# Optimization experiments

Measured on AMD Instinct MI355X. Metric: run time of the kernel, lower is better.

## Reference

```python
import jax, jax.numpy as jnp
import numpy as np

N_NODES = 50000
N_EDGES = 800000
N_GRAPHS = 256
N_FEAT, N_HID, N_EMB = 128, 256, 256
BN_EPS = 1e-5
W_SCALE = 0.05  # keep activations well-scaled through 3 layers


def setup_inputs() -> dict:
    key = jax.random.key(0)
    ks = jax.random.split(key, 9)
    x = jax.random.normal(ks[0], (N_NODES, N_FEAT), jnp.float32)
    edge_index = jax.random.randint(ks[1], (2, N_EDGES), 0, N_NODES)
    batch = jnp.sort(jax.random.randint(ks[2], (N_NODES,), 0, N_GRAPHS))
    return {
        "x": x,
        "edge_index": edge_index,
        "batch": batch,
        "W1_0": jax.random.normal(ks[3], (N_FEAT, N_HID), jnp.float32) * W_SCALE,
        "W2_0": jax.random.normal(ks[4], (N_HID, N_HID), jnp.float32) * W_SCALE,
        "gamma0": jnp.ones((N_HID,), jnp.float32),
        "beta0": jnp.zeros((N_HID,), jnp.float32),
        "W1_1": jax.random.normal(ks[5], (N_HID, N_HID), jnp.float32) * W_SCALE,
        "W2_1": jax.random.normal(ks[6], (N_HID, N_HID), jnp.float32) * W_SCALE,
        "gamma1": jnp.ones((N_HID,), jnp.float32),
        "beta1": jnp.zeros((N_HID,), jnp.float32),
        "W1_2": jax.random.normal(ks[7], (N_HID, N_HID), jnp.float32) * W_SCALE,
        "W2_2": jax.random.normal(ks[8], (N_HID, N_EMB), jnp.float32) * W_SCALE,
    }


def _gin_conv(x, src, dst, W1, W2):
    # PyG GINConv, eps=0: nn((1+eps)*x_i + sum_{j in N(i)} x_j)
    agg = jax.ops.segment_sum(x[src], dst, num_segments=N_NODES)  # [N, d]
    h = x + agg
    return jax.nn.relu(h @ W1) @ W2  # Linear(bias=False) -> act -> Linear(bias=False)


def _batch_norm(h, gamma, beta):
    # BatchNorm1d in training mode: biased batch stats over nodes
    mean = jnp.mean(h, axis=0)
    var = jnp.var(h, axis=0)
    return (h - mean) * jax.lax.rsqrt(var + BN_EPS) * gamma + beta


def reference(x, edge_index, batch, W1_0, W2_0, gamma0, beta0,
              W1_1, W2_1, gamma1, beta1, W1_2, W2_2):
    src, dst = edge_index[0], edge_index[1]
    layers = [(W1_0, W2_0, gamma0, beta0), (W1_1, W2_1, gamma1, beta1)]
    xs = []
    h = x
    for W1, W2, g, b in layers:  # n_layers-1 conv+act+BN blocks
        h = jax.nn.relu(_gin_conv(h, src, dst, W1, W2))
        h = _batch_norm(h, g, b)
        xs.append(h)
    h = _gin_conv(h, src, dst, W1_2, W2_2)  # final conv: no act, no BN
    xs.append(h)
    xpool = jax.ops.segment_sum(h, batch, num_segments=N_GRAPHS)  # global_add_pool
    return xpool, jnp.concatenate(xs, axis=1)
```

## Files before the change

kernel.cpp:

```cpp
#include <hip/hip_runtime.h>
#include <stdint.h>

typedef unsigned int u32;
typedef unsigned short u16;

using s16x8 = __attribute__((ext_vector_type(8))) short;
using f32x4 = __attribute__((ext_vector_type(4))) float;

#define N_NODES_C 50000
#define N_EDGES_C 800000
#define N_GRAPHS_C 256
#define N_FEAT_C 128
#define N_HID_C 256

static __device__ __forceinline__ float bf2f(u16 u) {
  union { u32 u; float f; } c; c.u = ((u32)u) << 16; return c.f;
}
static __device__ __forceinline__ u16 f2bf(float f) {
  union { float f; u32 u; } c; c.f = f;
  u32 u = c.u;
  return (u16)((u + 0x7fffu + ((u >> 16) & 1u)) >> 16);
}

static __device__ __forceinline__ void gload_lds16(const u16* g, u16* l) {
  __builtin_amdgcn_global_load_lds(
      (const __attribute__((address_space(1))) unsigned int*)g,
      (__attribute__((address_space(3))) unsigned int*)l, 16, 0, 0);
}

__global__ void convt_all_kernel(const float* __restrict__ Wa, const float* __restrict__ Wb,
                                 const float* __restrict__ Wc, const float* __restrict__ Wd,
                                 const float* __restrict__ We, const float* __restrict__ Wf,
                                 u16* oa, u16* ob, u16* oc, u16* od, u16* oe, u16* of_) {
  int m = blockIdx.y;
  const float* W; u16* o; int K;
  switch (m) {
    case 0: W = Wa; o = oa; K = 128; break;
    case 1: W = Wb; o = ob; K = 256; break;
    case 2: W = Wc; o = oc; K = 256; break;
    case 3: W = Wd; o = od; K = 256; break;
    case 4: W = We; o = oe; K = 256; break;
    default: W = Wf; o = of_; K = 256; break;
  }
  int idx = blockIdx.x * 256 + threadIdx.x;
  if (idx >= K * 256) return;
  int n = idx / K, k = idx - n * K;
  o[idx] = f2bf(W[(size_t)k * 256 + n]);
}

__global__ void cvt4_kernel(const float* __restrict__ x, u16* __restrict__ xb, int n4) {
  int idx = blockIdx.x * 256 + threadIdx.x;
  if (idx >= n4) return;
  float4 v = reinterpret_cast<const float4*>(x)[idx];
  u32 lo = (u32)f2bf(v.x) | ((u32)f2bf(v.y) << 16);
  u32 hi = (u32)f2bf(v.z) | ((u32)f2bf(v.w) << 16);
  uint2 w; w.x = lo; w.y = hi;
  reinterpret_cast<uint2*>(xb)[idx] = w;
}

__global__ void count_kernel(const int* __restrict__ dst, int* __restrict__ cnt, int E) {
  int e = blockIdx.x * 256 + threadIdx.x;
  if (e < E) atomicAdd(&cnt[dst[e]], 1);
}

__global__ void scanA_kernel(const int* __restrict__ cnt, int* __restrict__ incl,
                             int* __restrict__ bsum, int n) {
  __shared__ int sd[1024];
  int i = blockIdx.x * 1024 + (int)threadIdx.x;
  int v = (i < n) ? cnt[i] : 0;
  sd[threadIdx.x] = v;
  __syncthreads();
  for (int off = 1; off < 1024; off <<= 1) {
    int t = ((int)threadIdx.x >= off) ? sd[threadIdx.x - off] : 0;
    __syncthreads();
    sd[threadIdx.x] += t;
    __syncthreads();
  }
  if (i < n) incl[i] = sd[threadIdx.x];
  if (threadIdx.x == 1023) bsum[blockIdx.x] = sd[1023];
}

__global__ void scanB_kernel(int* bsum, int nb, float* stats0, float* stats1) {
  int t = threadIdx.x;
  for (int i = t; i < 512; i += 64) { stats0[i] = 0.f; stats1[i] = 0.f; }
  if (t == 0) {
    int s = 0;
    for (int b = 0; b < nb; b++) { int v = bsum[b]; bsum[b] = s; s += v; }
  }
}

__global__ void scanC_kernel(const int* __restrict__ cnt, const int* __restrict__ incl,
                             const int* __restrict__ bsum, int* __restrict__ offs,
                             int* __restrict__ cursor, int n) {
  int i = blockIdx.x * 1024 + (int)threadIdx.x;
  if (i < n) {
    int e = incl[i] - cnt[i] + bsum[blockIdx.x];
    offs[i] = e;
    cursor[i] = e;
  }
  if (i == 0) offs[n] = N_EDGES_C;
}

__global__ void fill_kernel(const int* __restrict__ src, const int* __restrict__ dst,
                            int* __restrict__ cursor, int* __restrict__ csr, int E) {
  int e = blockIdx.x * 256 + threadIdx.x;
  if (e < E) {
    int p = atomicAdd(&cursor[dst[e]], 1);
    csr[p] = src[e];
  }
}

template <int D>
__global__ __launch_bounds__(256) void agg_kernel(const u16* __restrict__ xin,
                                                  const int* __restrict__ offs,
                                                  const int* __restrict__ csr,
                                                  u16* __restrict__ hout) {
  constexpr int LPE = D / 8;
  constexpr int EPW = 64 / LPE;
  int wid = threadIdx.x >> 6, lane = threadIdx.x & 63;
  int node = blockIdx.x * 4 + wid;
  if (node >= N_NODES_C) return;
  int sub = lane / LPE;
  int fl = lane % LPE;
  int f0 = fl * 8;
  float acc[8];
  if (sub == 0) {
    uint4 v = *reinterpret_cast<const uint4*>(xin + (size_t)node * D + f0);
    const u32* pv = reinterpret_cast<const u32*>(&v);
#pragma unroll
    for (int t = 0; t < 4; t++) {
      acc[2 * t] = bf2f((u16)pv[t]);
      acc[2 * t + 1] = bf2f((u16)(pv[t] >> 16));
    }
  } else {
#pragma unroll
    for (int t = 0; t < 8; t++) acc[t] = 0.f;
  }
  int e = offs[node] + sub;
  int e1 = offs[node + 1];
  if (EPW == 2) {
    for (; e + 3 * EPW < e1; e += 4 * EPW) {
      int s0 = csr[e], s1 = csr[e + EPW], s2 = csr[e + 2 * EPW], s3 = csr[e + 3 * EPW];
      uint4 v0 = *reinterpret_cast<const uint4*>(xin + (size_t)s0 * D + f0);
      uint4 v1 = *reinterpret_cast<const uint4*>(xin + (size_t)s1 * D + f0);
      uint4 v2 = *reinterpret_cast<const uint4*>(xin + (size_t)s2 * D + f0);
      uint4 v3 = *reinterpret_cast<const uint4*>(xin + (size_t)s3 * D + f0);
      const u32* p0 = reinterpret_cast<const u32*>(&v0);
      const u32* p1 = reinterpret_cast<const u32*>(&v1);
      const u32* p2 = reinterpret_cast<const u32*>(&v2);
      const u32* p3 = reinterpret_cast<const u32*>(&v3);
#pragma unroll
      for (int t = 0; t < 4; t++) {
        acc[2 * t] += (bf2f((u16)p0[t]) + bf2f((u16)p1[t])) +
                      (bf2f((u16)p2[t]) + bf2f((u16)p3[t]));
        acc[2 * t + 1] += (bf2f((u16)(p0[t] >> 16)) + bf2f((u16)(p1[t] >> 16))) +
                          (bf2f((u16)(p2[t] >> 16)) + bf2f((u16)(p3[t] >> 16)));
      }
    }
  } else {
    for (; e + EPW < e1; e += 2 * EPW) {
      int s0 = csr[e], s1 = csr[e + EPW];
      uint4 v0 = *reinterpret_cast<const uint4*>(xin + (size_t)s0 * D + f0);
      uint4 v1 = *reinterpret_cast<const uint4*>(xin + (size_t)s1 * D + f0);
      const u32* p0 = reinterpret_cast<const u32*>(&v0);
      const u32* p1 = reinterpret_cast<const u32*>(&v1);
#pragma unroll
      for (int t = 0; t < 4; t++) {
        acc[2 * t] += bf2f((u16)p0[t]) + bf2f((u16)p1[t]);
        acc[2 * t + 1] += bf2f((u16)(p0[t] >> 16)) + bf2f((u16)(p1[t] >> 16));
      }
    }
  }
  for (; e < e1; e += EPW) {
    int s = csr[e];
    uint4 v = *reinterpret_cast<const uint4*>(xin + (size_t)s * D + f0);
    const u32* pv = reinterpret_cast<const u32*>(&v);
#pragma unroll
    for (int t = 0; t < 4; t++) {
      acc[2 * t] += bf2f((u16)pv[t]);
      acc[2 * t + 1] += bf2f((u16)(pv[t] >> 16));
    }
  }
#pragma unroll
  for (int j = 0; j < 8; j++) {
    if (EPW == 4) acc[j] += __shfl_xor(acc[j], 16, 64);
    acc[j] += __shfl_xor(acc[j], 32, 64);
  }
  if (sub == 0) {
    u32 w[4];
#pragma unroll
    for (int t = 0; t < 4; t++)
      w[t] = (u32)f2bf(acc[2 * t]) | ((u32)f2bf(acc[2 * t + 1]) << 16);
    *reinterpret_cast<uint4*>(hout + (size_t)node * D + f0) =
        *reinterpret_cast<const uint4*>(w);
  }
}

template <int K, bool RELU, bool OUTF32, bool STATS>
__global__ __launch_bounds__(256, 4) void gemm_kernel(const u16* __restrict__ A,
                                                      const u16* __restrict__ Bt,
                                                      u16* __restrict__ outB,
                                                      float* __restrict__ outF, int ldc,
                                                      float* __restrict__ statsp) {
  constexpr int BM = 64, BK = 64;
  __shared__ u16 Al[BM * BK];
  __shared__ u16 Bl[256 * BK];
  const int tid = threadIdx.x;
  const int wid = tid >> 6, lane = tid & 63;
  const int brow = blockIdx.x * BM;
  const int wc = wid * 64;
  f32x4 acc[4][4] = {};

  const int lrow = lane >> 3;
  const int lw = lane & 7;
  const int colA = (lw ^ lrow) * 8;
  const int sw = (lane & 7) << 3;

  for (int k0 = 0; k0 < K; k0 += BK) {
#pragma unroll
    for (int i = 0; i < 10; i++) {
      int c = wid * 10 + i;
      if (c < 8) {
        int r = c * 8 + lrow;
        int gr = brow + r;
        gr = gr < N_NODES_C ? gr : N_NODES_C - 1;
        gload_lds16(A + (size_t)gr * K + k0 + colA, &Al[c * 512]);
      } else {
        int cc = c - 8;
        int r = cc * 8 + lrow;
        gload_lds16(Bt + (size_t)r * K + k0 + colA, &Bl[cc * 512]);
      }
    }
    __syncthreads();
#pragma unroll
    for (int ks = 0; ks < BK; ks += 32) {
      const int kk = ks + (lane >> 4) * 8;
      const int ki = kk ^ sw;
      s16x8 a[4], b[4];
#pragma unroll
      for (int m = 0; m < 4; m++)
        a[m] = *reinterpret_cast<const s16x8*>(&Al[(m * 16 + (lane & 15)) * 64 + ki]);
#pragma unroll
      for (int n = 0; n < 4; n++)
        b[n] = *reinterpret_cast<const s16x8*>(&Bl[(wc + n * 16 + (lane & 15)) * 64 + ki]);
#pragma unroll
      for (int m = 0; m < 4; m++)
#pragma unroll
        for (int n = 0; n < 4; n++)
          acc[m][n] = __builtin_amdgcn_mfma_f32_16x16x32_bf16(a[m], b[n], acc[m][n], 0, 0, 0);
    }
    __syncthreads();
  }

  const int cb = wc + (lane & 15);
  const int rsub = (lane >> 4) * 4;
  float s1[4] = {0.f, 0.f, 0.f, 0.f}, s2[4] = {0.f, 0.f, 0.f, 0.f};
#pragma unroll
  for (int m = 0; m < 4; m++) {
#pragma unroll
    for (int r = 0; r < 4; r++) {
      int row = brow + m * 16 + rsub + r;
      if (row >= N_NODES_C) continue;
#pragma unroll
      for (int n = 0; n < 4; n++) {
        float v = acc[m][n][r];
        if (RELU) v = v > 0.f ? v : 0.f;
        int col = cb + n * 16;
        if (OUTF32)
          outF[(size_t)row * ldc + col] = v;
        else
          outB[(size_t)row * ldc + col] = f2bf(v);
        if (STATS) { s1[n] += v; s2[n] += v * v; }
      }
    }
  }
  if (STATS) {
#pragma unroll
    for (int n = 0; n < 4; n++) {
      float a0 = s1[n], b0 = s2[n];
      a0 += __shfl_xor(a0, 16, 64);
      b0 += __shfl_xor(b0, 16, 64);
      a0 += __shfl_xor(a0, 32, 64);
      b0 += __shfl_xor(b0, 32, 64);
      if (lane < 16) {
        atomicAdd(&statsp[cb + n * 16], a0);
        atomicAdd(&statsp[256 + cb + n * 16], b0);
      }
    }
  }
}

__global__ __launch_bounds__(256) void norm_kernel(const u16* __restrict__ xp,
                                                   const float* __restrict__ stats,
                                                   const float* __restrict__ gamma,
                                                   const float* __restrict__ beta,
                                                   float* __restrict__ cout,
                                                   u16* __restrict__ xn) {
  const float invM = 1.0f / (float)N_NODES_C;
  int f0 = (threadIdx.x & 127) * 2;
  int half = threadIdx.x >> 7;
  float m0 = stats[f0] * invM, m1 = stats[f0 + 1] * invM;
  float v0 = stats[256 + f0] * invM - m0 * m0;
  float v1 = stats[256 + f0 + 1] * invM - m1 * m1;
  float sc0 = gamma[f0] * rsqrtf(v0 + 1e-5f);
  float sc1 = gamma[f0 + 1] * rsqrtf(v1 + 1e-5f);
  float bi0 = beta[f0] - m0 * sc0;
  float bi1 = beta[f0 + 1] - m1 * sc1;
  for (int r = blockIdx.x * 2 + half; r < N_NODES_C; r += 2 * gridDim.x) {
    u32 w = *reinterpret_cast<const u32*>(xp + (size_t)r * 256 + f0);
    float y0 = fmaf(bf2f((u16)w), sc0, bi0);
    float y1 = fmaf(bf2f((u16)(w >> 16)), sc1, bi1);
    float2 y; y.x = y0; y.y = y1;
    *reinterpret_cast<float2*>(cout + (size_t)r * 768 + f0) = y;
    *reinterpret_cast<u32*>(xn + (size_t)r * 256 + f0) =
        (u32)f2bf(y0) | ((u32)f2bf(y1) << 16);
  }
}

__global__ __launch_bounds__(256) void pool_kernel(const float* __restrict__ c, int ldc,
                                                   const int* __restrict__ batch,
                                                   float* __restrict__ outp) {
  __shared__ float red[1024];
  int g = blockIdx.x;
  int wid = threadIdx.x >> 6, lane = threadIdx.x & 63;
  int lo = 0, hi = N_NODES_C;
  while (lo < hi) { int mid = (lo + hi) >> 1; if (batch[mid] < g) lo = mid + 1; else hi = mid; }
  int start = lo;
  hi = N_NODES_C;
  while (lo < hi) { int mid = (lo + hi) >> 1; if (batch[mid] <= g) lo = mid + 1; else hi = mid; }
  int end = lo;
  float acc[4] = {0.f, 0.f, 0.f, 0.f};
  for (int r = start + wid; r < end; r += 4) {
    float4 v = *reinterpret_cast<const float4*>(c + (size_t)r * ldc + lane * 4);
    acc[0] += v.x; acc[1] += v.y; acc[2] += v.z; acc[3] += v.w;
  }
#pragma unroll
  for (int j = 0; j < 4; j++) red[wid * 256 + lane * 4 + j] = acc[j];
  __syncthreads();
  int f = threadIdx.x;
  float s = red[f] + red[256 + f] + red[512 + f] + red[768 + f];
  outp[(size_t)g * 256 + f] = s;
}

extern "C" void kernel_launch(void* const* d_in, const int* in_sizes, int n_in,
                              void* d_out, int out_size, void* d_ws, size_t ws_size,
                              hipStream_t stream) {
  (void)in_sizes; (void)n_in; (void)out_size; (void)ws_size;
  const float* x = (const float*)d_in[0];
  const int* ei = (const int*)d_in[1];
  const int* batch = (const int*)d_in[2];
  const float* W1_0 = (const float*)d_in[3];
  const float* W2_0 = (const float*)d_in[4];
  const float* gamma0 = (const float*)d_in[5];
  const float* beta0 = (const float*)d_in[6];
  const float* W1_1 = (const float*)d_in[7];
  const float* W2_1 = (const float*)d_in[8];
  const float* gamma1 = (const float*)d_in[9];
  const float* beta1 = (const float*)d_in[10];
  const float* W1_2 = (const float*)d_in[11];
  const float* W2_2 = (const float*)d_in[12];

  float* out = (float*)d_out;
  float* xpool = out;
  float* concat = out + (size_t)N_GRAPHS_C * N_HID_C;

  char* ws = (char*)d_ws;
  size_t off = 0;
  auto alloc = [&](size_t bytes) -> char* {
    char* p = ws + off;
    off = (off + bytes + 255) & ~(size_t)255;
    return p;
  };
  int* cnt = (int*)alloc((N_NODES_C + 1) * 4);
  int* offs = (int*)alloc((N_NODES_C + 1) * 4);
  int* cursor = (int*)alloc(N_NODES_C * 4);
  int* incl = (int*)alloc(N_NODES_C * 4);
  int* bsum = (int*)alloc(64 * 4);
  int* csr = (int*)alloc((size_t)N_EDGES_C * 4);
  u16* xb = (u16*)alloc((size_t)N_NODES_C * N_FEAT_C * 2);
  u16* hin = (u16*)alloc((size_t)N_NODES_C * N_HID_C * 2);
  u16* tbuf = (u16*)alloc((size_t)N_NODES_C * N_HID_C * 2);
  u16* xn = (u16*)alloc((size_t)N_NODES_C * N_HID_C * 2);
  u16* w10t = (u16*)alloc((size_t)N_FEAT_C * N_HID_C * 2);
  u16* w20t = (u16*)alloc((size_t)N_HID_C * N_HID_C * 2);
  u16* w11t = (u16*)alloc((size_t)N_HID_C * N_HID_C * 2);
  u16* w21t = (u16*)alloc((size_t)N_HID_C * N_HID_C * 2);
  u16* w12t = (u16*)alloc((size_t)N_HID_C * N_HID_C * 2);
  u16* w22t = (u16*)alloc((size_t)N_HID_C * N_HID_C * 2);
  float* stats0 = (float*)alloc(512 * 4);
  float* stats1 = (float*)alloc(512 * 4);

  const int* srcv = ei;
  const int* dstv = ei + N_EDGES_C;
  const int nb = (N_NODES_C + 1023) / 1024;
  const int ggrid = (N_NODES_C + 63) / 64;

  hipMemsetAsync(cnt, 0, (N_NODES_C + 1) * 4, stream);

  convt_all_kernel<<<dim3(256, 6), 256, 0, stream>>>(W1_0, W2_0, W1_1, W2_1, W1_2, W2_2,
                                                     w10t, w20t, w11t, w21t, w12t, w22t);
  cvt4_kernel<<<(N_NODES_C * N_FEAT_C / 4 + 255) / 256, 256, 0, stream>>>(
      x, xb, N_NODES_C * N_FEAT_C / 4);

  count_kernel<<<(N_EDGES_C + 255) / 256, 256, 0, stream>>>(dstv, cnt, N_EDGES_C);
  scanA_kernel<<<nb, 1024, 0, stream>>>(cnt, incl, bsum, N_NODES_C);
  scanB_kernel<<<1, 64, 0, stream>>>(bsum, nb, stats0, stats1);
  scanC_kernel<<<nb, 1024, 0, stream>>>(cnt, incl, bsum, offs, cursor, N_NODES_C);
  fill_kernel<<<(N_EDGES_C + 255) / 256, 256, 0, stream>>>(srcv, dstv, cursor, csr, N_EDGES_C);

  agg_kernel<128><<<(N_NODES_C + 3) / 4, 256, 0, stream>>>(xb, offs, csr, hin);
  gemm_kernel<128, true, false, false><<<ggrid, 256, 0, stream>>>(hin, w10t, tbuf, nullptr, N_HID_C, nullptr);
  gemm_kernel<256, true, false, true><<<ggrid, 256, 0, stream>>>(tbuf, w20t, hin, nullptr, N_HID_C, stats0);
  norm_kernel<<<2048, 256, 0, stream>>>(hin, stats0, gamma0, beta0, concat + 0, xn);

  agg_kernel<256><<<(N_NODES_C + 3) / 4, 256, 0, stream>>>(xn, offs, csr, hin);
  gemm_kernel<256, true, false, false><<<ggrid, 256, 0, stream>>>(hin, w11t, tbuf, nullptr, N_HID_C, nullptr);
  gemm_kernel<256, true, false, true><<<ggrid, 256, 0, stream>>>(tbuf, w21t, hin, nullptr, N_HID_C, stats1);
  norm_kernel<<<2048, 256, 0, stream>>>(hin, stats1, gamma1, beta1, concat + 256, xn);

  agg_kernel<256><<<(N_NODES_C + 3) / 4, 256, 0, stream>>>(xn, offs, csr, hin);
  gemm_kernel<256, true, false, false><<<ggrid, 256, 0, stream>>>(hin, w12t, tbuf, nullptr, N_HID_C, nullptr);
  gemm_kernel<256, false, true, false><<<ggrid, 256, 0, stream>>>(tbuf, w22t, nullptr, concat + 512, 768, nullptr);

  pool_kernel<<<N_GRAPHS_C, 256, 0, stream>>>(concat + 512, 768, batch, xpool);
}
```

Measured before the change: 483.6 us.

## Fold BatchNorm affine into aggregation and enlarge GEMM tile to 128 rows

After: 455.2 us. 5.9% less time.

```diff
diff --git a/kernel.cpp b/kernel.cpp
--- a/kernel.cpp
+++ b/kernel.cpp
@@ -110,10 +110,11 @@
   }
 }
 
-template <int D>
+template <int D, bool AFFINE>
 __global__ __launch_bounds__(256) void agg_kernel(const u16* __restrict__ xin,
                                                   const int* __restrict__ offs,
                                                   const int* __restrict__ csr,
+                                                  const float* __restrict__ sb,
                                                   u16* __restrict__ hout) {
   constexpr int LPE = D / 8;
   constexpr int EPW = 64 / LPE;
@@ -136,8 +137,9 @@
 #pragma unroll
     for (int t = 0; t < 8; t++) acc[t] = 0.f;
   }
-  int e = offs[node] + sub;
+  int e0 = offs[node];
   int e1 = offs[node + 1];
+  int e = e0 + sub;
   if (EPW == 2) {
     for (; e + 3 * EPW < e1; e += 4 * EPW) {
       int s0 = csr[e], s1 = csr[e + EPW], s2 = csr[e + 2 * EPW], s3 = csr[e + 3 * EPW];
@@ -187,6 +189,17 @@
     acc[j] += __shfl_xor(acc[j], 32, 64);
   }
   if (sub == 0) {
+    if (AFFINE) {
+      float dp1 = (float)(e1 - e0 + 1);
+      float4 sca = *reinterpret_cast<const float4*>(sb + f0);
+      float4 scb = *reinterpret_cast<const float4*>(sb + f0 + 4);
+      float4 bia = *reinterpret_cast<const float4*>(sb + 256 + f0);
+      float4 bib = *reinterpret_cast<const float4*>(sb + 256 + f0 + 4);
+      float sc[8] = {sca.x, sca.y, sca.z, sca.w, scb.x, scb.y, scb.z, scb.w};
+      float bi[8] = {bia.x, bia.y, bia.z, bia.w, bib.x, bib.y, bib.z, bib.w};
+#pragma unroll
+      for (int j = 0; j < 8; j++) acc[j] = fmaf(acc[j], sc[j], bi[j] * dp1);
+    }
     u32 w[4];
 #pragma unroll
     for (int t = 0; t < 4; t++)
@@ -197,18 +210,19 @@
 }
 
 template <int K, bool RELU, bool OUTF32, bool STATS>
-__global__ __launch_bounds__(256, 4) void gemm_kernel(const u16* __restrict__ A,
+__global__ __launch_bounds__(512, 2) void gemm_kernel(const u16* __restrict__ A,
                                                       const u16* __restrict__ Bt,
                                                       u16* __restrict__ outB,
                                                       float* __restrict__ outF, int ldc,
                                                       float* __restrict__ statsp) {
-  constexpr int BM = 64, BK = 64;
+  constexpr int BM = 128, BK = 64;
   __shared__ u16 Al[BM * BK];
   __shared__ u16 Bl[256 * BK];
   const int tid = threadIdx.x;
   const int wid = tid >> 6, lane = tid & 63;
   const int brow = blockIdx.x * BM;
-  const int wc = wid * 64;
+  const int wr = (wid >> 2) * 64;
+  const int wc = (wid & 3) * 64;
   f32x4 acc[4][4] = {};
 
   const int lrow = lane >> 3;
@@ -218,15 +232,15 @@
 
   for (int k0 = 0; k0 < K; k0 += BK) {
 #pragma unroll
-    for (int i = 0; i < 10; i++) {
-      int c = wid * 10 + i;
-      if (c < 8) {
+    for (int i = 0; i < 6; i++) {
+      int c = wid * 6 + i;
+      if (c < 16) {
         int r = c * 8 + lrow;
         int gr = brow + r;
         gr = gr < N_NODES_C ? gr : N_NODES_C - 1;
         gload_lds16(A + (size_t)gr * K + k0 + colA, &Al[c * 512]);
       } else {
-        int cc = c - 8;
+        int cc = c - 16;
         int r = cc * 8 + lrow;
         gload_lds16(Bt + (size_t)r * K + k0 + colA, &Bl[cc * 512]);
       }
@@ -239,7 +253,7 @@
       s16x8 a[4], b[4];
 #pragma unroll
       for (int m = 0; m < 4; m++)
-        a[m] = *reinterpret_cast<const s16x8*>(&Al[(m * 16 + (lane & 15)) * 64 + ki]);
+        a[m] = *reinterpret_cast<const s16x8*>(&Al[(wr + m * 16 + (lane & 15)) * 64 + ki]);
 #pragma unroll
       for (int n = 0; n < 4; n++)
         b[n] = *reinterpret_cast<const s16x8*>(&Bl[(wc + n * 16 + (lane & 15)) * 64 + ki]);
@@ -259,7 +273,7 @@
   for (int m = 0; m < 4; m++) {
 #pragma unroll
     for (int r = 0; r < 4; r++) {
-      int row = brow + m * 16 + rsub + r;
+      int row = brow + wr + m * 16 + rsub + r;
       if (row >= N_NODES_C) continue;
 #pragma unroll
       for (int n = 0; n < 4; n++) {
@@ -295,7 +309,7 @@
                                                    const float* __restrict__ gamma,
                                                    const float* __restrict__ beta,
                                                    float* __restrict__ cout,
-                                                   u16* __restrict__ xn) {
+                                                   float* __restrict__ sb) {
   const float invM = 1.0f / (float)N_NODES_C;
   int f0 = (threadIdx.x & 127) * 2;
   int half = threadIdx.x >> 7;
@@ -306,14 +320,16 @@
   float sc1 = gamma[f0 + 1] * rsqrtf(v1 + 1e-5f);
   float bi0 = beta[f0] - m0 * sc0;
   float bi1 = beta[f0 + 1] - m1 * sc1;
+  if (blockIdx.x == 0 && half == 0) {
+    sb[f0] = sc0; sb[f0 + 1] = sc1;
+    sb[256 + f0] = bi0; sb[256 + f0 + 1] = bi1;
+  }
   for (int r = blockIdx.x * 2 + half; r < N_NODES_C; r += 2 * gridDim.x) {
     u32 w = *reinterpret_cast<const u32*>(xp + (size_t)r * 256 + f0);
     float y0 = fmaf(bf2f((u16)w), sc0, bi0);
     float y1 = fmaf(bf2f((u16)(w >> 16)), sc1, bi1);
     float2 y; y.x = y0; y.y = y1;
     *reinterpret_cast<float2*>(cout + (size_t)r * 768 + f0) = y;
-    *reinterpret_cast<u32*>(xn + (size_t)r * 256 + f0) =
-        (u32)f2bf(y0) | ((u32)f2bf(y1) << 16);
   }
 }
 
@@ -380,7 +396,7 @@
   u16* xb = (u16*)alloc((size_t)N_NODES_C * N_FEAT_C * 2);
   u16* hin = (u16*)alloc((size_t)N_NODES_C * N_HID_C * 2);
   u16* tbuf = (u16*)alloc((size_t)N_NODES_C * N_HID_C * 2);
-  u16* xn = (u16*)alloc((size_t)N_NODES_C * N_HID_C * 2);
+  u16* hpre = (u16*)alloc((size_t)N_NODES_C * N_HID_C * 2);
   u16* w10t = (u16*)alloc((size_t)N_FEAT_C * N_HID_C * 2);
   u16* w20t = (u16*)alloc((size_t)N_HID_C * N_HID_C * 2);
   u16* w11t = (u16*)alloc((size_t)N_HID_C * N_HID_C * 2);
@@ -389,11 +405,13 @@
   u16* w22t = (u16*)alloc((size_t)N_HID_C * N_HID_C * 2);
   float* stats0 = (float*)alloc(512 * 4);
   float* stats1 = (float*)alloc(512 * 4);
+  float* sb0 = (float*)alloc(512 * 4);
+  float* sb1 = (float*)alloc(512 * 4);
 
   const int* srcv = ei;
   const int* dstv = ei + N_EDGES_C;
   const int nb = (N_NODES_C + 1023) / 1024;
-  const int ggrid = (N_NODES_C + 63) / 64;
+  const int ggrid = (N_NODES_C + 127) / 128;
 
   hipMemsetAsync(cnt, 0, (N_NODES_C + 1) * 4, stream);
 
@@ -408,19 +426,19 @@
   scanC_kernel<<<nb, 1024, 0, stream>>>(cnt, incl, bsum, offs, cursor, N_NODES_C);
   fill_kernel<<<(N_EDGES_C + 255) / 256, 256, 0, stream>>>(srcv, dstv, cursor, csr, N_EDGES_C);
 
-  agg_kernel<128><<<(N_NODES_C + 3) / 4, 256, 0, stream>>>(xb, offs, csr, hin);
-  gemm_kernel<128, true, false, false><<<ggrid, 256, 0, stream>>>(hin, w10t, tbuf, nullptr, N_HID_C, nullptr);
-  gemm_kernel<256, true, false, true><<<ggrid, 256, 0, stream>>>(tbuf, w20t, hin, nullptr, N_HID_C, stats0);
-  norm_kernel<<<2048, 256, 0, stream>>>(hin, stats0, gamma0, beta0, concat + 0, xn);
-
-  agg_kernel<256><<<(N_NODES_C + 3) / 4, 256, 0, stream>>>(xn, offs, csr, hin);
-  gemm_kernel<256, true, false, false><<<ggrid, 256, 0, stream>>>(hin, w11t, tbuf, nullptr, N_HID_C, nullptr);
-  gemm_kernel<256, true, false, true><<<ggrid, 256, 0, stream>>>(tbuf, w21t, hin, nullptr, N_HID_C, stats1);
-  norm_kernel<<<2048, 256, 0, stream>>>(hin, stats1, gamma1, beta1, concat + 256, xn);
-
-  agg_kernel<256><<<(N_NODES_C + 3) / 4, 256, 0, stream>>>(xn, offs, csr, hin);
-  gemm_kernel<256, true, false, false><<<ggrid, 256, 0, stream>>>(hin, w12t, tbuf, nullptr, N_HID_C, nullptr);
-  gemm_kernel<256, false, true, false><<<ggrid, 256, 0, stream>>>(tbuf, w22t, nullptr, concat + 512, 768, nullptr);
+  agg_kernel<128, false><<<(N_NODES_C + 3) / 4, 256, 0, stream>>>(xb, offs, csr, nullptr, hin);
+  gemm_kernel<128, true, false, false><<<ggrid, 512, 0, stream>>>(hin, w10t, tbuf, nullptr, N_HID_C, nullptr);
+  gemm_kernel<256, true, false, true><<<ggrid, 512, 0, stream>>>(tbuf, w20t, hpre, nullptr, N_HID_C, stats0);
+  norm_kernel<<<2048, 256, 0, stream>>>(hpre, stats0, gamma0, beta0, concat + 0, sb0);
+
+  agg_kernel<256, true><<<(N_NODES_C + 3) / 4, 256, 0, stream>>>(hpre, offs, csr, sb0, hin);
+  gemm_kernel<256, true, false, false><<<ggrid, 512, 0, stream>>>(hin, w11t, tbuf, nullptr, N_HID_C, nullptr);
+  gemm_kernel<256, true, false, true><<<ggrid, 512, 0, stream>>>(tbuf, w21t, hpre, nullptr, N_HID_C, stats1);
+  norm_kernel<<<2048, 256, 0, stream>>>(hpre, stats1, gamma1, beta1, concat + 256, sb1);
+
+  agg_kernel<256, true><<<(N_NODES_C + 3) / 4, 256, 0, stream>>>(hpre, offs, csr, sb1, hin);
+  gemm_kernel<256, true, false, false><<<ggrid, 512, 0, stream>>>(hin, w12t, tbuf, nullptr, N_HID_C, nullptr);
+  gemm_kernel<256, false, true, false><<<ggrid, 512, 0, stream>>>(tbuf, w22t, nullptr, concat + 512, 768, nullptr);
 
   pool_kernel<<<N_GRAPHS_C, 256, 0, stream>>>(concat + 512, 768, batch, xpool);
 }
```
